# Kernel tuning notes

Hardware: AMD Instinct MI355X
Metric: run time of the kernel (lower is better)

## Reference

```python
import jax, jax.numpy as jnp
import numpy as np


def _quant8(w):
    # Brevitas Int8 per-tensor weight quant: scale = max|w|/127, round, clip, dequant.
    s = jnp.max(jnp.abs(w)) / 127.0
    q = jnp.clip(jnp.round(w / s), -127.0, 127.0) * s
    # straight-through estimator (matches brevitas backward)
    return w + jax.lax.stop_gradient(q - w)


def _conv1d(x, w, b):
    # x: [B, Cin, L], w: [Cout, Cin, K]
    y = jax.lax.conv_general_dilated(x, w, window_strides=(1,), padding='VALID',
                                     dimension_numbers=('NCW', 'OIW', 'NCW'))
    return y + b[None, :, None]


def _maxpool2(x):
    B, C, L = x.shape
    L2 = L // 2
    return jnp.max(x[:, :, :2 * L2].reshape(B, C, L2, 2), axis=-1)


def _lrelu(x):
    return jnp.where(x > 0, x, 0.1 * x)


def setup_inputs() -> dict:
    key = jax.random.key(0)
    ks = jax.random.split(key, 13)
    B, C, L = 32768, 2, 128
    flat = 32 * 27  # 864, from tracing conv/pool stack at L=128
    d = {
        'x': jax.random.normal(ks[0], (B, C, L), dtype=jnp.float32),
        'w1': jax.random.normal(ks[1], (16, 2, 2), dtype=jnp.float32) * 0.3,
        'b1': jax.random.normal(ks[2], (16,), dtype=jnp.float32) * 0.05,
        'w2': jax.random.normal(ks[3], (16, 16, 3), dtype=jnp.float32) * 0.1,
        'b2': jax.random.normal(ks[4], (16,), dtype=jnp.float32) * 0.05,
        'w3': jax.random.normal(ks[5], (32, 16, 5), dtype=jnp.float32) * 0.1,
        'b3': jax.random.normal(ks[6], (32,), dtype=jnp.float32) * 0.05,
        'w4': jax.random.normal(ks[7], (32, 32, 5), dtype=jnp.float32) * 0.08,
        'b4': jax.random.normal(ks[8], (32,), dtype=jnp.float32) * 0.05,
        'wd': jax.random.normal(ks[9], (64, flat), dtype=jnp.float32) * 0.03,
        'bd': jax.random.normal(ks[10], (64,), dtype=jnp.float32) * 0.05,
        'wo': jax.random.normal(ks[11], (1, 64), dtype=jnp.float32) * 0.1,
        'bo': jax.random.normal(ks[12], (1,), dtype=jnp.float32) * 0.05,
    }
    return d


def reference(x, w1, b1, w2, b2, w3, b3, w4, b4, wd, bd, wo, bo):
    h = _lrelu(_conv1d(x, _quant8(w1), b1))        # [B,16,127]
    h = _lrelu(_conv1d(h, _quant8(w2), b2))        # [B,16,125]
    h = _maxpool2(h)                               # [B,16,62]
    h = _lrelu(_conv1d(h, _quant8(w3), b3))        # [B,32,58]
    h = _lrelu(_conv1d(h, _quant8(w4), b4))        # [B,32,54]
    h = _maxpool2(h)                               # [B,32,27]
    h = h.reshape(h.shape[0], -1)                  # [B,864]
    h = _lrelu(h @ _quant8(wd).T + bd)             # [B,64]
    return h @ _quant8(wo).T + bo                  # [B,1]
```

## Files before the change

### kernel.cpp

```cpp
#include <hip/hip_runtime.h>
#include <hip/hip_bf16.h>

typedef __hip_bfloat16 bf16;
typedef _Float16 h16;
typedef __attribute__((ext_vector_type(8))) _Float16 h16x8;
typedef __attribute__((ext_vector_type(4))) float f32x4;
typedef __attribute__((ext_vector_type(16))) float f32x16;

__device__ __forceinline__ float lrelu(float x) { return fmaxf(x, 0.1f * x); }
__device__ __forceinline__ float ldE(const void* p, long i, int f32) {
    return f32 ? ((const float*)p)[i] : __bfloat162float(((const bf16*)p)[i]);
}
__device__ __forceinline__ uint2 pack4(float a, float b, float c, float d) {
    union { _Float16 h[4]; uint2 u; } t;
    t.h[0] = (_Float16)a; t.h[1] = (_Float16)b; t.h[2] = (_Float16)c; t.h[3] = (_Float16)d;
    return t.u;
}
__device__ __forceinline__ unsigned umx(unsigned a, unsigned b) { return a > b ? a : b; }
#define LDS_FENCE() asm volatile("" ::: "memory")


__device__ __forceinline__ float qv(const void* src, int idx, float sc, int f32) {
    float w = ldE(src, idx, f32);
    float q = rintf(w / sc);
    return fminf(127.f, fmaxf(-127.f, q)) * sc;
}

__device__ float block_scale(const void* src, int n, int f32, int tid, float* red) {
    unsigned m = 0;
    const uint4* p = (const uint4*)src;
    if (f32) {
        int nv = n >> 2;
        for (int i = tid; i < nv; i += 256) {
            uint4 u = p[i];
            m = umx(m, u.x & 0x7FFFFFFFu); m = umx(m, u.y & 0x7FFFFFFFu);
            m = umx(m, u.z & 0x7FFFFFFFu); m = umx(m, u.w & 0x7FFFFFFFu);
        }
        union { unsigned u; float f; } c; c.u = m;
        red[tid] = c.f;
    } else {
        int nv = n >> 3;
        for (int i = tid; i < nv; i += 256) {
            uint4 u = p[i];
            unsigned a;
            a = u.x & 0x7FFF7FFFu; m = umx(m, a >> 16); m = umx(m, a & 0xFFFFu);
            a = u.y & 0x7FFF7FFFu; m = umx(m, a >> 16); m = umx(m, a & 0xFFFFu);
            a = u.z & 0x7FFF7FFFu; m = umx(m, a >> 16); m = umx(m, a & 0xFFFFu);
            a = u.w & 0x7FFF7FFFu; m = umx(m, a >> 16); m = umx(m, a & 0xFFFFu);
        }
        union { unsigned u; float f; } c; c.u = m << 16;
        red[tid] = c.f;
    }
    __syncthreads();
    for (int s = 128; s > 0; s >>= 1) {
        if (tid < s) red[tid] = fmaxf(red[tid], red[tid + s]);
        __syncthreads();
    }
    float r = red[0] / 127.f;
    __syncthreads();
    return r;
}

__global__ void __launch_bounds__(256) prep(
    const unsigned short* __restrict__ xu,
    const void* __restrict__ w1, const void* __restrict__ w2,
    const void* __restrict__ w3, const void* __restrict__ w4,
    const void* __restrict__ wd, const void* __restrict__ wo,
    const void* __restrict__ b1, const void* __restrict__ b2,
    const void* __restrict__ b3, const void* __restrict__ b4,
    const void* __restrict__ bd, const void* __restrict__ bo,
    float* __restrict__ wsf)
{
    int tid = threadIdx.x, which = blockIdx.x;
    __shared__ float red[256];
    __shared__ int cnt;
    if (tid == 0) cnt = 0;
    __syncthreads();
    int bad = 0;
    for (int i = tid; i < 2048; i += 256) {
        int e = (xu[i] >> 7) & 0xFF;
        if (e >= 147) bad = 1;
    }
    atomicAdd(&cnt, bad);
    __syncthreads();
    const int f32 = (cnt > 4) ? 1 : 0;
    h16* wh = (h16*)(wsf + 292);

    if (which < 216) {
        float sc = block_scale(wd, 55296, f32, tid, red);
        int s = which * 256 + tid;
        int o = s / 864, r = s - o * 864;
        int cch = r / 27, i = r - cch * 27;
        int mt = o >> 4;
        int e = ((mt * 27 + i) * 64 + (o & 15) + (cch >> 3) * 16) * 8 + (cch & 7);
        wh[8704 + e] = (h16)qv(wd, s, sc, f32);
    } else if (which == 216) {
        float s1 = block_scale(w1, 64, f32, tid, red);
        float s2 = block_scale(w2, 768, f32, tid, red);
        for (int e = tid; e < 512; e += 256)  wh[64000 + e] = (h16)0.f;
        for (int e = tid; e < 1024; e += 256) wh[e] = (h16)0.f;
        __syncthreads();
        if (tid < 64) {
            int s = tid, co = s >> 2, ci = (s >> 1) & 1, dk = s & 1;
            wh[64000 + (co + dk * 16) * 8 + ci] = (h16)qv(w1, s, s1, f32);
        }
        for (int s = tid; s < 768; s += 256) {
            int mm = s / 48, r = s - mm * 48;
            int ci = r / 3, dk = r - ci * 3;
            int k = dk * 16 + ci;
            int e = (k >> 5) * 512 + (mm + ((k >> 3) & 3) * 16) * 8 + (k & 7);
            wh[e] = (h16)qv(w2, s, s2, f32);
        }
    } else if (which == 217) {
        float sc = block_scale(w3, 2560, f32, tid, red);
        for (int s = tid; s < 2560; s += 256) {
            int mm = s / 80, r = s - mm * 80;
            int ci = r / 5, dk = r - ci * 5;
            int e = (dk * 64 + mm + (ci >> 3) * 32) * 8 + (ci & 7);
            wh[1024 + e] = (h16)qv(w3, s, sc, f32);
        }
    } else if (which == 218) {
        float sc = block_scale(w4, 5120, f32, tid, red);
        for (int s = tid; s < 5120; s += 256) {
            int mm = s / 160, r = s - mm * 160;
            int ci = r / 5, dk = r - ci * 5;
            int k = dk * 32 + ci;
            int e = (k >> 4) * 512 + (mm + ((k >> 3) & 1) * 32) * 8 + (k & 7);
            wh[3584 + e] = (h16)qv(w4, s, sc, f32);
        }
    } else {
        float sc = block_scale(wo, 64, f32, tid, red);
        if (tid < 64) wsf[224 + tid] = qv(wo, tid, sc, f32);
        if (tid < 16)        wsf[64 + tid]        = ldE(b1, tid, f32);
        else if (tid < 32)   wsf[80 + tid - 16]   = ldE(b2, tid - 16, f32);
        else if (tid < 64)   wsf[96 + tid - 32]   = ldE(b3, tid - 32, f32);
        else if (tid < 96)   wsf[128 + tid - 64]  = ldE(b4, tid - 64, f32);
        else if (tid < 160)  wsf[160 + tid - 96]  = ldE(bd, tid - 96, f32);
        else if (tid == 160) wsf[288]             = ldE(bo, 0, f32);
        if (tid == 0) ((int*)wsf)[290] = f32;
    }
}

__global__ void __launch_bounds__(256, 2) qcnn_main(
    const void* __restrict__ x,
    const float* __restrict__ wsf,
    void* __restrict__ out)
{
    const int f32flag = ((const int*)wsf)[290];
    const h16*  wh  = (const h16*)(wsf + 292);
    const h16*  F2g = wh;
    const h16*  F3g = wh + 1024;
    const h16*  F4g = wh + 3584;
    const h16*  FDg = wh + 8704;
    const h16*  F1g = wh + 64000;

    __shared__ __align__(16) h16 Uall[4][2112];
    __shared__ __align__(16) h16 Vall[4][2208];
    __shared__ __align__(16) h16 flatb[8][872];
    __shared__ float red[256];

    int tid  = threadIdx.x;
    int lane = tid & 63;
    int w    = __builtin_amdgcn_readfirstlane(tid >> 6);
    int n16  = lane & 15, kg16 = (lane >> 4) & 3;
    int n32  = lane & 31, kg32 = (lane >> 5) & 1;
    int o16  = kg16 * 4;
    h16* U = Uall[w];
    h16* V = Vall[w];
    long b0 = (long)blockIdx.x * 8;

    h16x8 a1, a2[2], a3[5], a4[10];
    a1 = *(const h16x8*)&F1g[lane * 8];
#pragma unroll
    for (int c = 0; c < 2; ++c)  a2[c] = *(const h16x8*)&F2g[c * 512 + lane * 8];
#pragma unroll
    for (int c = 0; c < 5; ++c)  a3[c] = *(const h16x8*)&F3g[c * 512 + lane * 8];
#pragma unroll
    for (int c = 0; c < 10; ++c) a4[c] = *(const h16x8*)&F4g[c * 512 + lane * 8];
    f32x4 b1v = *(const f32x4*)&wsf[64 + o16];
    f32x4 b2v = *(const f32x4*)&wsf[80 + o16];

    const h16 hz = (h16)0.f;
    const h16x8 zrow = {hz, hz, hz, hz, hz, hz, hz, hz};

    for (int it = 0; it < 2; ++it) {
        int slot = w * 2 + it;
        long sb = (b0 + slot) * 256;

        LDS_FENCE();
        {
            float x00 = ldE(x, sb + lane, f32flag);
            float x10 = ldE(x, sb + 128 + lane, f32flag);
            float x01 = ldE(x, sb + 64 + lane, f32flag);
            float x11 = ldE(x, sb + 192 + lane, f32flag);
            h16x8 r0 = zrow, r1 = zrow;
            r0[0] = (h16)x00; r0[1] = (h16)x10;
            r1[0] = (h16)x01; r1[1] = (h16)x11;
            *(h16x8*)&V[lane * 8]        = r0;
            *(h16x8*)&V[(64 + lane) * 8] = r1;
            if (lane < 3) *(h16x8*)&V[(128 + lane) * 8] = zrow;
        }
        LDS_FENCE();

#pragma unroll
        for (int t = 0; t < 8; ++t) {
            int n = t * 16 + n16;
            f32x4 acc = b1v;
            h16x8 bfr = *(const h16x8*)&V[(n + kg16) * 8];
            acc = __builtin_amdgcn_mfma_f32_16x16x32_f16(a1, bfr, acc, 0, 0, 0);
            if (n < 127) {
                uint2 p = pack4(lrelu(acc[0]), lrelu(acc[1]), lrelu(acc[2]), lrelu(acc[3]));
                *(uint2*)&U[(o16 >> 3) * 1056 + n * 8 + (o16 & 7)] = p;
            }
        }
        if (lane < 8) {
            int g = lane & 1, row = 127 + (lane >> 1);
            *(uint4*)&U[g * 1056 + row * 8] = make_uint4(0, 0, 0, 0);
        }
        LDS_FENCE();

#pragma unroll
        for (int t = 0; t < 8; ++t) {
            int n = t * 16 + n16;
            f32x4 acc = b2v;
#pragma unroll
            for (int c = 0; c < 2; ++c) {
                int k0 = c * 32 + kg16 * 8;
                int dk = k0 >> 4, g = (k0 & 15) >> 3;
                h16x8 bfr = *(const h16x8*)&U[g * 1056 + (n + dk) * 8];
                acc = __builtin_amdgcn_mfma_f32_16x16x32_f16(a2[c], bfr, acc, 0, 0, 0);
            }
            if (n < 125) {
                uint2 p = pack4(lrelu(acc[0]), lrelu(acc[1]), lrelu(acc[2]), lrelu(acc[3]));
                *(uint2*)&V[(o16 >> 3) * 1008 + n * 8 + (o16 & 7)] = p;
            }
        }
        LDS_FENCE();

        if (lane < 62) {
#pragma unroll
            for (int g = 0; g < 2; ++g) {
                h16x8 pa = *(const h16x8*)&V[g * 1008 + (2 * lane) * 8];
                h16x8 pb = *(const h16x8*)&V[g * 1008 + (2 * lane + 1) * 8];
                h16x8 mm;
#pragma unroll
                for (int e = 0; e < 8; ++e) mm[e] = pa[e] > pb[e] ? pa[e] : pb[e];
                *(h16x8*)&U[g * 1056 + lane * 8] = mm;
            }
        }
        LDS_FENCE();

#pragma unroll
        for (int t = 0; t < 2; ++t) {
            int n = t * 32 + n32;
            f32x16 acc = {0.f,0.f,0.f,0.f,0.f,0.f,0.f,0.f,0.f,0.f,0.f,0.f,0.f,0.f,0.f,0.f};
#pragma unroll
            for (int c = 0; c < 5; ++c) {
                h16x8 bfr = *(const h16x8*)&U[kg32 * 1056 + (n + c) * 8];
                acc = __builtin_amdgcn_mfma_f32_32x32x16_f16(a3[c], bfr, acc, 0, 0, 0);
            }
            if (n < 58) {
#pragma unroll
                for (int g = 0; g < 4; ++g) {
                    int r0 = 8 * g + 4 * kg32;
                    f32x4 bv = *(const f32x4*)&wsf[96 + r0];
                    uint2 p = pack4(lrelu(acc[4*g+0] + bv[0]), lrelu(acc[4*g+1] + bv[1]),
                                    lrelu(acc[4*g+2] + bv[2]), lrelu(acc[4*g+3] + bv[3]));
                    *(uint2*)&V[g * 552 + n * 8 + 4 * kg32] = p;
                }
            }
        }
        LDS_FENCE();

#pragma unroll
        for (int t = 0; t < 2; ++t) {
            int n = t * 32 + n32;
            f32x16 acc = {0.f,0.f,0.f,0.f,0.f,0.f,0.f,0.f,0.f,0.f,0.f,0.f,0.f,0.f,0.f,0.f};
#pragma unroll
            for (int c = 0; c < 10; ++c) {
                int k0 = c * 16 + kg32 * 8;
                int dk = k0 >> 5, g = (k0 >> 3) & 3;
                h16x8 bfr = *(const h16x8*)&V[g * 552 + (n + dk) * 8];
                acc = __builtin_amdgcn_mfma_f32_32x32x16_f16(a4[c], bfr, acc, 0, 0, 0);
            }
            if (n < 54) {
#pragma unroll
                for (int g = 0; g < 4; ++g) {
                    int r0 = 8 * g + 4 * kg32;
                    f32x4 bv = *(const f32x4*)&wsf[128 + r0];
                    uint2 p = pack4(lrelu(acc[4*g+0] + bv[0]), lrelu(acc[4*g+1] + bv[1]),
                                    lrelu(acc[4*g+2] + bv[2]), lrelu(acc[4*g+3] + bv[3]));
                    *(uint2*)&U[g * 448 + n * 8 + 4 * kg32] = p;
                }
            }
        }
        LDS_FENCE();

        if (lane < 27) {
#pragma unroll
            for (int g = 0; g < 4; ++g) {
                h16x8 pa = *(const h16x8*)&U[g * 448 + (2 * lane) * 8];
                h16x8 pb = *(const h16x8*)&U[g * 448 + (2 * lane + 1) * 8];
                h16x8 mm;
#pragma unroll
                for (int e = 0; e < 8; ++e) mm[e] = pa[e] > pb[e] ? pa[e] : pb[e];
                *(h16x8*)&flatb[slot][(g * 27 + lane) * 8] = mm;
            }
        }
    }
    __syncthreads();

    int o0g = w * 16 + o16;
    f32x4 dacc = *(const f32x4*)&wsf[160 + o0g];
    for (int c = 0; c < 27; ++c) {
        h16x8 aw = *(const h16x8*)&FDg[((w * 27 + c) * 64 + lane) * 8];
        h16x8 bh = *(const h16x8*)&flatb[lane & 7][(kg16 * 27 + c) * 8];
        dacc = __builtin_amdgcn_mfma_f32_16x16x32_f16(aw, bh, dacc, 0, 0, 0);
    }
    f32x4 qov = *(const f32x4*)&wsf[224 + o0g];
    float part = 0.f;
#pragma unroll
    for (int q = 0; q < 4; ++q) part += lrelu(dacc[q]) * qov[q];
    red[tid] = part;
    __syncthreads();
    if (tid < 8) {
        float y = wsf[288];
#pragma unroll
        for (int g = 0; g < 16; ++g) y += red[(g >> 2) * 64 + (g & 3) * 16 + tid];
        if (f32flag) ((float*)out)[b0 + tid] = y;
        else         ((bf16*)out)[b0 + tid] = __float2bfloat16(y);
    }
}

extern "C" void kernel_launch(void* const* d_in, const int* in_sizes, int n_in,
                              void* d_out, int out_size, void* d_ws, size_t ws_size,
                              hipStream_t stream) {
    const void* x  = d_in[0];
    const void* w1 = d_in[1];
    const void* b1 = d_in[2];
    const void* w2 = d_in[3];
    const void* b2 = d_in[4];
    const void* w3 = d_in[5];
    const void* b3 = d_in[6];
    const void* w4 = d_in[7];
    const void* b4 = d_in[8];
    const void* wd = d_in[9];
    const void* bd = d_in[10];
    const void* wo = d_in[11];
    const void* bo = d_in[12];
    float* wsf = (float*)d_ws;

    int B = in_sizes[0] / 256;
    prep<<<220, 256, 0, stream>>>((const unsigned short*)x,
                                  w1, w2, w3, w4, wd, wo,
                                  b1, b2, b3, b4, bd, bo, wsf);
    qcnn_main<<<B / 8, 256, 0, stream>>>(x, wsf, d_out);
}
```

Before: 194.7 us.

## Prefetch inputs, fold conv biases into MFMA accumulators, split pool buffers by parity

Both per-slot input loads are hoisted ahead of the slot loop, so global-memory latency for the second slot overlaps the first slot's compute. The conv3 and conv4 biases are preloaded into the accumulator registers instead of being read from shared weight memory and added in the epilogue. Conv2 and conv4 outputs are now written to LDS in even/odd-split order, so the max-pool reads contiguous strided-by-one rows instead of stride-2 pairs, which should cut LDS bank conflicts. Conv4's U buffer stride grows from 448 to 512 elements, which must still fit the existing LDS allocation, and the extra live registers raise register pressure.

```diff
diff --git a/kernel.cpp b/kernel.cpp
--- a/kernel.cpp
+++ b/kernel.cpp
@@ -179,23 +179,37 @@
     for (int c = 0; c < 10; ++c) a4[c] = *(const h16x8*)&F4g[c * 512 + lane * 8];
     f32x4 b1v = *(const f32x4*)&wsf[64 + o16];
     f32x4 b2v = *(const f32x4*)&wsf[80 + o16];
+    f32x16 c3i, c4i;
+#pragma unroll
+    for (int g = 0; g < 4; ++g) {
+        f32x4 bv3 = *(const f32x4*)&wsf[96 + 8 * g + 4 * kg32];
+        f32x4 bv4 = *(const f32x4*)&wsf[128 + 8 * g + 4 * kg32];
+#pragma unroll
+        for (int q = 0; q < 4; ++q) { c3i[4*g+q] = bv3[q]; c4i[4*g+q] = bv4[q]; }
+    }
 
     const h16 hz = (h16)0.f;
     const h16x8 zrow = {hz, hz, hz, hz, hz, hz, hz, hz};
 
+    float xl[2][4];
+#pragma unroll
+    for (int it = 0; it < 2; ++it) {
+        long sb = (b0 + w * 2 + it) * 256;
+        xl[it][0] = ldE(x, sb + lane, f32flag);
+        xl[it][1] = ldE(x, sb + 128 + lane, f32flag);
+        xl[it][2] = ldE(x, sb + 64 + lane, f32flag);
+        xl[it][3] = ldE(x, sb + 192 + lane, f32flag);
+    }
+
+#pragma unroll
     for (int it = 0; it < 2; ++it) {
         int slot = w * 2 + it;
-        long sb = (b0 + slot) * 256;
 
         LDS_FENCE();
         {
-            float x00 = ldE(x, sb + lane, f32flag);
-            float x10 = ldE(x, sb + 128 + lane, f32flag);
-            float x01 = ldE(x, sb + 64 + lane, f32flag);
-            float x11 = ldE(x, sb + 192 + lane, f32flag);
             h16x8 r0 = zrow, r1 = zrow;
-            r0[0] = (h16)x00; r0[1] = (h16)x10;
-            r1[0] = (h16)x01; r1[1] = (h16)x11;
+            r0[0] = (h16)xl[it][0]; r0[1] = (h16)xl[it][1];
+            r1[0] = (h16)xl[it][2]; r1[1] = (h16)xl[it][3];
             *(h16x8*)&V[lane * 8]        = r0;
             *(h16x8*)&V[(64 + lane) * 8] = r1;
             if (lane < 3) *(h16x8*)&V[(128 + lane) * 8] = zrow;
@@ -231,8 +245,9 @@
                 acc = __builtin_amdgcn_mfma_f32_16x16x32_f16(a2[c], bfr, acc, 0, 0, 0);
             }
             if (n < 125) {
+                int ph = (n & 1) * 64 + (n >> 1);
                 uint2 p = pack4(lrelu(acc[0]), lrelu(acc[1]), lrelu(acc[2]), lrelu(acc[3]));
-                *(uint2*)&V[(o16 >> 3) * 1008 + n * 8 + (o16 & 7)] = p;
+                *(uint2*)&V[(o16 >> 3) * 1008 + ph * 8 + (o16 & 7)] = p;
             }
         }
         LDS_FENCE();
@@ -240,8 +255,8 @@
         if (lane < 62) {
 #pragma unroll
             for (int g = 0; g < 2; ++g) {
-                h16x8 pa = *(const h16x8*)&V[g * 1008 + (2 * lane) * 8];
-                h16x8 pb = *(const h16x8*)&V[g * 1008 + (2 * lane + 1) * 8];
+                h16x8 pa = *(const h16x8*)&V[g * 1008 + lane * 8];
+                h16x8 pb = *(const h16x8*)&V[g * 1008 + (64 + lane) * 8];
                 h16x8 mm;
 #pragma unroll
                 for (int e = 0; e < 8; ++e) mm[e] = pa[e] > pb[e] ? pa[e] : pb[e];
@@ -253,7 +268,7 @@
 #pragma unroll
         for (int t = 0; t < 2; ++t) {
             int n = t * 32 + n32;
-            f32x16 acc = {0.f,0.f,0.f,0.f,0.f,0.f,0.f,0.f,0.f,0.f,0.f,0.f,0.f,0.f,0.f,0.f};
+            f32x16 acc = c3i;
 #pragma unroll
             for (int c = 0; c < 5; ++c) {
                 h16x8 bfr = *(const h16x8*)&U[kg32 * 1056 + (n + c) * 8];
@@ -262,10 +277,8 @@
             if (n < 58) {
 #pragma unroll
                 for (int g = 0; g < 4; ++g) {
-                    int r0 = 8 * g + 4 * kg32;
-                    f32x4 bv = *(const f32x4*)&wsf[96 + r0];
-                    uint2 p = pack4(lrelu(acc[4*g+0] + bv[0]), lrelu(acc[4*g+1] + bv[1]),
-                                    lrelu(acc[4*g+2] + bv[2]), lrelu(acc[4*g+3] + bv[3]));
+                    uint2 p = pack4(lrelu(acc[4*g+0]), lrelu(acc[4*g+1]),
+                                    lrelu(acc[4*g+2]), lrelu(acc[4*g+3]));
                     *(uint2*)&V[g * 552 + n * 8 + 4 * kg32] = p;
                 }
             }
@@ -275,7 +288,7 @@
 #pragma unroll
         for (int t = 0; t < 2; ++t) {
             int n = t * 32 + n32;
-            f32x16 acc = {0.f,0.f,0.f,0.f,0.f,0.f,0.f,0.f,0.f,0.f,0.f,0.f,0.f,0.f,0.f,0.f};
+            f32x16 acc = c4i;
 #pragma unroll
             for (int c = 0; c < 10; ++c) {
                 int k0 = c * 16 + kg32 * 8;
@@ -284,13 +297,12 @@
                 acc = __builtin_amdgcn_mfma_f32_32x32x16_f16(a4[c], bfr, acc, 0, 0, 0);
             }
             if (n < 54) {
+                int ph = (n & 1) * 32 + (n >> 1);
 #pragma unroll
                 for (int g = 0; g < 4; ++g) {
-                    int r0 = 8 * g + 4 * kg32;
-                    f32x4 bv = *(const f32x4*)&wsf[128 + r0];
-                    uint2 p = pack4(lrelu(acc[4*g+0] + bv[0]), lrelu(acc[4*g+1] + bv[1]),
-                                    lrelu(acc[4*g+2] + bv[2]), lrelu(acc[4*g+3] + bv[3]));
-                    *(uint2*)&U[g * 448 + n * 8 + 4 * kg32] = p;
+                    uint2 p = pack4(lrelu(acc[4*g+0]), lrelu(acc[4*g+1]),
+                                    lrelu(acc[4*g+2]), lrelu(acc[4*g+3]));
+                    *(uint2*)&U[g * 512 + ph * 8 + 4 * kg32] = p;
                 }
             }
         }
@@ -299,8 +311,8 @@
         if (lane < 27) {
 #pragma unroll
             for (int g = 0; g < 4; ++g) {
-                h16x8 pa = *(const h16x8*)&U[g * 448 + (2 * lane) * 8];
-                h16x8 pb = *(const h16x8*)&U[g * 448 + (2 * lane + 1) * 8];
+                h16x8 pa = *(const h16x8*)&U[g * 512 + lane * 8];
+                h16x8 pb = *(const h16x8*)&U[g * 512 + (32 + lane) * 8];
                 h16x8 mm;
 #pragma unroll
                 for (int e = 0; e < 8; ++e) mm[e] = pa[e] > pb[e] ? pa[e] : pb[e];
```

After: 191.9 us. About the same (-1.4%).
